# Optimization experiments

Hardware: AMD Instinct MI355X
Metric: run time of the kernel (lower is better)

The kernel has to match this reference:

```python
import jax, jax.numpy as jnp
import numpy as np

B, S, C, L, E, A, H = 4, 4, 4, 512, 64, 32, 8


def _xavier(k, shape, fan_in, fan_out):
    lim = float(np.sqrt(6.0 / (fan_in + fan_out)))
    return jax.random.uniform(k, shape, jnp.float32, -lim, lim)


def setup_inputs() -> dict:
    key = jax.random.key(0)
    ks = jax.random.split(key, 14)
    inp = {
        "query_sequences": jax.random.normal(ks[0], (B, S, L, E), jnp.float32),
        "key_sequences": jax.random.normal(ks[1], (B, S, L, E), jnp.float32),
        "value_sequences": jax.random.normal(ks[2], (B, S, L, E), jnp.float32),
        "query_constants": jax.random.normal(ks[3], (B, C, 1, E), jnp.float32),
        "key_constants": jax.random.normal(ks[4], (B, C, 1, E), jnp.float32),
        "value_constants": jax.random.normal(ks[5], (B, C, 1, E), jnp.float32),
        "qw_seq": _xavier(ks[6], (S, H, E, A), E, A),
        "kw_seq": _xavier(ks[7], (S, H, E, A), E, A),
        "vw_seq": _xavier(ks[8], (S, H, E, A), E, A),
        "qw_con": _xavier(ks[9], (C, H, E, A), E, A),
        "kw_con": _xavier(ks[10], (C, H, E, A), E, A),
        "vw_con": _xavier(ks[11], (C, H, E, A), E, A),
        "head_w_seq": _xavier(ks[12], (S, H * A, E), H * A, E),
        "head_w_con": _xavier(ks[13], (C, H * A, E), H * A, E),
        "mask": 1,
    }
    return inp


def reference(query_sequences, key_sequences, value_sequences,
              query_constants, key_constants, value_constants,
              qw_seq, kw_seq, vw_seq, qw_con, kw_con, vw_con,
              head_w_seq, head_w_con, mask):
    # Per-sequence / per-constant, per-head QKV projections
    q_s = jnp.einsum('bsle,shea->bshla', query_sequences, qw_seq)      # [B,S,H,L,A]
    q_c = jnp.einsum('bcle,chea->bchla', query_constants, qw_con)      # [B,C,H,1,A]
    k_s = jnp.einsum('bsle,shea->bhsla', key_sequences, kw_seq).reshape(B, H, S * L, A)
    k_c = jnp.einsum('bcle,chea->bhcla', key_constants, kw_con).reshape(B, H, C, A)
    v_s = jnp.einsum('bsle,shea->bhsla', value_sequences, vw_seq).reshape(B, H, S * L, A)
    v_c = jnp.einsum('bcle,chea->bhcla', value_constants, vw_con).reshape(B, H, C, A)
    k_all = jnp.concatenate([k_s, k_c], axis=2)                        # [B,H,K,A], K=S*L+C
    v_all = jnp.concatenate([v_s, v_c], axis=2)

    scale = 1.0 / jnp.sqrt(jnp.asarray(A, jnp.float32))
    scores_s = jnp.einsum('bshla,bhka->bshlk', q_s, k_all) * scale     # [B,S,H,L,K]
    if mask:
        # block-causal: within each of the S key blocks mask future timesteps;
        # constant columns (time index -1) are always visible.
        kt = jnp.concatenate([jnp.tile(jnp.arange(L), S), jnp.full((C,), -1)])
        m = kt[None, :] > jnp.arange(L)[:, None]                       # [L,K]
        scores_s = jnp.where(m, -jnp.inf, scores_s)
    p_s = jax.nn.softmax(scores_s, axis=-1)
    out_s = jnp.einsum('bshlk,bhka->bslha', p_s, v_all).reshape(B, S, L, H * A)
    seq_out = jnp.einsum('bslf,sfe->bsle', out_s, head_w_seq)          # [B,S,L,E]

    scores_c = jnp.einsum('bchla,bhka->bchlk', q_c, k_all) * scale     # [B,C,H,1,K]
    p_c = jax.nn.softmax(scores_c, axis=-1)
    out_c = jnp.einsum('bchlk,bhka->bclha', p_c, v_all).reshape(B, C, 1, H * A)
    con_out = jnp.einsum('bclf,cfe->bcle', out_c, head_w_con)          # [B,C,1,E]
    return (seq_out, con_out)
```

## Files before the change

### kernel.cpp

```cpp
#include <hip/hip_runtime.h>
#include <hip/hip_bf16.h>

#define B_ 4
#define S_ 4
#define C_ 4
#define L_ 512
#define E_ 64
#define A_ 32
#define H_ 8
#define HA_ 256
#define KREAL 2052
#define KP 2112
#define NKT 33
#define SCALE 0.17677669529663687f
#define SCALE2 0.25503486321392056f
#define NEGINF (-__builtin_inff())

using bf16  = __bf16;
using bf16x8 = __attribute__((ext_vector_type(8))) __bf16;
using f32x4  = __attribute__((ext_vector_type(4))) float;

#define OFF_QS    0ull
#define OFF_KALL  4194304ull
#define OFF_VT    8519680ull
#define OFF_OUTS  12845056ull
#define OFF_OUTC  17039360ull

__device__ __forceinline__ bool detect_f32(const unsigned int* __restrict__ x0,
                                           int* sh_cnt)
{
  if (threadIdx.x == 0) *sh_cnt = 0;
  __syncthreads();
  int weird = 0;
  for (int i = threadIdx.x; i < 1024; i += blockDim.x) {
    unsigned h = x0[i] & 0xffffu;
    int e = (int)((h >> 7) & 0xFF);
    if (e == 0xFF || e < 0x60 || e > 0x9F) weird++;
  }
  atomicAdd(sh_cnt, weird);
  __syncthreads();
  int cnt = *sh_cnt;
  return __builtin_amdgcn_readfirstlane(cnt) > 256;
}

__device__ __forceinline__ bf16x8 ld8(const void* p, size_t idx, bool isf32) {
  if (isf32) {
    const float* f = (const float*)p + idx;
    float4 lo = *(const float4*)f;
    float4 hi = *(const float4*)(f + 4);
    bf16x8 v;
    v[0] = (bf16)lo.x; v[1] = (bf16)lo.y; v[2] = (bf16)lo.z; v[3] = (bf16)lo.w;
    v[4] = (bf16)hi.x; v[5] = (bf16)hi.y; v[6] = (bf16)hi.z; v[7] = (bf16)hi.w;
    return v;
  }
  return *(const bf16x8*)((const bf16*)p + idx);
}
__device__ __forceinline__ float ldf(const void* p, size_t idx, bool isf32) {
  return isf32 ? ((const float*)p)[idx] : (float)((const bf16*)p)[idx];
}

__global__ __launch_bounds__(256) void proj_kernel(
    const void* __restrict__ xq, const void* __restrict__ xk, const void* __restrict__ xv,
    const void* __restrict__ kc_in, const void* __restrict__ vc_in,
    const void* __restrict__ wq, const void* __restrict__ wk, const void* __restrict__ wv,
    const void* __restrict__ wkc, const void* __restrict__ wvc,
    bf16* __restrict__ qs, bf16* __restrict__ kall, bf16* __restrict__ vt)
{
  __shared__ int sh_cnt;
  bool isf32 = detect_f32((const unsigned int*)xq, &sh_cnt);
  int bid = blockIdx.x;
  int tid = threadIdx.x;
  if (bid < 256) {
    int b = bid >> 6, s = (bid >> 4) & 3, h = (bid >> 1) & 7, lc = bid & 1;
    __shared__ bf16 wt[3 * 32 * 72];
    __shared__ bf16 v_lds[32 * 264];
    {
      size_t hb = (size_t)(s * H_ + h) * E_ * A_;
      int e = tid >> 2, ac = tid & 3;
      bf16x8 vq = ld8(wq, hb + e * 32 + ac * 8, isf32);
      bf16x8 vk = ld8(wk, hb + e * 32 + ac * 8, isf32);
      bf16x8 vv = ld8(wv, hb + e * 32 + ac * 8, isf32);
#pragma unroll
      for (int j = 0; j < 8; ++j) {
        int a = ac * 8 + j;
        wt[0 * 2304 + a * 72 + e] = vq[j];
        wt[1 * 2304 + a * 72 + e] = vk[j];
        wt[2 * 2304 + a * 72 + e] = vv[j];
      }
    }
    __syncthreads();
    int lane = tid & 63, wave = tid >> 6;
    int quad = lane >> 4, r = lane & 15;
    bf16x8 bq[2][2], bk[2][2], bv[2][2];
#pragma unroll
    for (int kc = 0; kc < 2; ++kc)
#pragma unroll
      for (int nt = 0; nt < 2; ++nt) {
        int off = (nt * 16 + r) * 72 + kc * 32 + quad * 8;
        bq[kc][nt] = *(const bf16x8*)&wt[off];
        bk[kc][nt] = *(const bf16x8*)&wt[2304 + off];
        bv[kc][nt] = *(const bf16x8*)&wt[4608 + off];
      }
    const size_t xbase = (size_t)(b * S_ + s) * L_ * E_;
    const size_t qsb   = (size_t)((b * S_ + s) * H_ + h) * L_ * A_;
    const size_t kab   = (size_t)(b * H_ + h) * KP * A_;
    const size_t vtb   = (size_t)(b * H_ + h) * A_ * KP;
#pragma unroll 1
    for (int i = 0; i < 4; ++i) {
      int lloc0 = (wave * 4 + i) * 16;
      int row0 = lc * 256 + lloc0;
      size_t rowoff = xbase + (size_t)(row0 + r) * E_ + quad * 8;
      bf16x8 aq0 = ld8(xq, rowoff, isf32);
      bf16x8 aq1 = ld8(xq, rowoff + 32, isf32);
      bf16x8 ak0 = ld8(xk, rowoff, isf32);
      bf16x8 ak1 = ld8(xk, rowoff + 32, isf32);
      bf16x8 av0 = ld8(xv, rowoff, isf32);
      bf16x8 av1 = ld8(xv, rowoff + 32, isf32);
#pragma unroll
      for (int nt = 0; nt < 2; ++nt) {
        f32x4 accq = {0.f,0.f,0.f,0.f}, acck = {0.f,0.f,0.f,0.f}, accv = {0.f,0.f,0.f,0.f};
        accq = __builtin_amdgcn_mfma_f32_16x16x32_bf16(aq0, bq[0][nt], accq, 0,0,0);
        accq = __builtin_amdgcn_mfma_f32_16x16x32_bf16(aq1, bq[1][nt], accq, 0,0,0);
        acck = __builtin_amdgcn_mfma_f32_16x16x32_bf16(ak0, bk[0][nt], acck, 0,0,0);
        acck = __builtin_amdgcn_mfma_f32_16x16x32_bf16(ak1, bk[1][nt], acck, 0,0,0);
        accv = __builtin_amdgcn_mfma_f32_16x16x32_bf16(av0, bv[0][nt], accv, 0,0,0);
        accv = __builtin_amdgcn_mfma_f32_16x16x32_bf16(av1, bv[1][nt], accv, 0,0,0);
#pragma unroll
        for (int reg = 0; reg < 4; ++reg) {
          int l = row0 + quad * 4 + reg;
          int a = nt * 16 + r;
          qs[qsb + (size_t)l * A_ + a]              = (bf16)(accq[reg] * SCALE2);
          kall[kab + (size_t)(s * L_ + l) * A_ + a] = (bf16)acck[reg];
          v_lds[a * 264 + lloc0 + quad * 4 + reg]   = (bf16)accv[reg];
        }
      }
    }
    __syncthreads();
    {
      int a = tid >> 3, c8 = tid & 7;
      size_t rb = vtb + (size_t)a * KP + s * L_ + lc * 256;
#pragma unroll
      for (int j = 0; j < 4; ++j) {
        int chunk = j * 8 + c8;
        *(bf16x8*)&vt[rb + chunk * 8] = *(const bf16x8*)&v_lds[a * 264 + chunk * 8];
      }
    }
  } else {
    int cid = bid - 256;
    int b = cid >> 5, c = (cid >> 3) & 3, h = cid & 7;
    if (tid < 32) {
      int a = tid;
      float kacc = 0.f, vacc = 0.f;
#pragma unroll 8
      for (int e = 0; e < E_; ++e) {
        float xke = ldf(kc_in, (b * C_ + c) * E_ + e, isf32);
        float xve = ldf(vc_in, (b * C_ + c) * E_ + e, isf32);
        float wke = ldf(wkc, ((size_t)(c * H_ + h) * E_ + e) * A_ + a, isf32);
        float wve = ldf(wvc, ((size_t)(c * H_ + h) * E_ + e) * A_ + a, isf32);
        kacc += xke * wke;
        vacc += xve * wve;
      }
      kall[((size_t)(b * H_ + h) * KP + (S_ * L_ + c)) * A_ + a] = (bf16)kacc;
      vt[((size_t)(b * H_ + h) * A_ + a) * KP + (S_ * L_ + c)]   = (bf16)vacc;
    }
    if (c == 0) {
      for (int idx = tid; idx < 60 * 32; idx += 256) {
        int k = KREAL + (idx >> 5), a = idx & 31;
        kall[((size_t)(b * H_ + h) * KP + k) * A_ + a] = (bf16)0.f;
        vt[((size_t)(b * H_ + h) * A_ + a) * KP + k]   = (bf16)0.f;
      }
    }
  }
}

__global__ __launch_bounds__(256) void attn_kernel(
    const bf16* __restrict__ qs, const bf16* __restrict__ kall, const bf16* __restrict__ vt,
    const int* __restrict__ maskp, bf16* __restrict__ outs,
    const void* __restrict__ qc_raw, const void* __restrict__ wqc_raw,
    const unsigned int* __restrict__ x0, float* __restrict__ outc)
{
  __shared__ __attribute__((aligned(16))) bf16 kt_lds[64 * 40];
  __shared__ __attribute__((aligned(16))) bf16 vt_lds[32 * 72];
  __shared__ __attribute__((aligned(16))) bf16 p_lds[4 * 16 * 72];
  __shared__ int sh_cnt;
  int bid = blockIdx.x, tid = threadIdx.x;
  int lane = tid & 63, wave = tid >> 6, quad = lane >> 4, r = lane & 15;
  if (bid < 1024) {
    int h = bid & 7;
    int q0 = (bid >> 3) & 7;
    int s = (bid >> 6) & 3;
    int b = (bid >> 8) & 3;
    int base = (q0 + 2 * (b >> 1)) & 7;
    int qt = (b & 1) ? 7 - base : base;
    bool causal = (*maskp != 0);
    int wrow = qt * 64 + wave * 16;
    int lrow = wrow + r;
    int blockmax = qt * 64 + 63;

    const size_t qsb = (size_t)((b * S_ + s) * H_ + h) * L_ * A_;
    bf16x8 aq = *(const bf16x8*)&qs[qsb + (size_t)(wrow + r) * A_ + quad * 8];

    f32x4 o[2];
    { f32x4 z = {0.f,0.f,0.f,0.f}; o[0] = z; o[1] = z; }
    float l_run = 0.f;

    const size_t kbase = (size_t)(b * H_ + h) * KP * A_;
    const size_t vbase = (size_t)(b * H_ + h) * A_ * KP;
    const int pbase = wave * 16 * 72;

#pragma unroll 1
    for (int kt = 0; kt < NKT; ++kt) {
      int kmod = (kt & 7) * 64;
      if (causal && kt < 32 && kmod > blockmax) continue;
      __syncthreads();
      {
        int krow = tid >> 2, c4 = tid & 3;
        *(bf16x8*)&kt_lds[krow * 40 + c4 * 8] =
            *(const bf16x8*)&kall[kbase + (size_t)(kt * 64 + krow) * A_ + c4 * 8];
        int a8 = tid >> 3, c8 = tid & 7;
        *(bf16x8*)&vt_lds[a8 * 72 + c8 * 8] =
            *(const bf16x8*)&vt[vbase + (size_t)a8 * KP + kt * 64 + c8 * 8];
      }
      __syncthreads();
      if (causal && kt < 32 && kmod >= wrow + 16) continue;
      bool fullv = (kt < 32) && (!causal || kmod + 63 <= wrow);

      f32x4 sf[4];
#pragma unroll
      for (int kg = 0; kg < 4; ++kg) {
        bf16x8 ka = *(const bf16x8*)&kt_lds[(kg * 16 + r) * 40 + quad * 8];
        f32x4 z = {0.f,0.f,0.f,0.f};
        sf[kg] = __builtin_amdgcn_mfma_f32_16x16x32_bf16(ka, aq, z, 0,0,0);
      }
      if (!fullv) {
        int thresh = (kt < 32) ? (lrow - kmod) : 3;
#pragma unroll
        for (int kg = 0; kg < 4; ++kg)
#pragma unroll
          for (int reg = 0; reg < 4; ++reg)
            if (kg * 16 + quad * 4 + reg > thresh) sf[kg][reg] = NEGINF;
      }
      float psum = 0.f;
#pragma unroll
      for (int kg = 0; kg < 4; ++kg) {
        float p0 = exp2f(sf[kg][0]);
        float p1 = exp2f(sf[kg][1]);
        float p2 = exp2f(sf[kg][2]);
        float p3 = exp2f(sf[kg][3]);
        psum += (p0 + p1) + (p2 + p3);
        union { bf16 hh[4]; uint2 u2; } pk;
        pk.hh[0] = (bf16)p0; pk.hh[1] = (bf16)p1; pk.hh[2] = (bf16)p2; pk.hh[3] = (bf16)p3;
        *(uint2*)&p_lds[pbase + r * 72 + kg * 16 + quad * 4] = pk.u2;
      }
      psum += __shfl_xor(psum, 16);
      psum += __shfl_xor(psum, 32);
      l_run += psum;
#pragma unroll
      for (int kc2 = 0; kc2 < 2; ++kc2) {
        bf16x8 ap = *(const bf16x8*)&p_lds[pbase + r * 72 + kc2 * 32 + quad * 8];
#pragma unroll
        for (int nt = 0; nt < 2; ++nt) {
          bf16x8 bv = *(const bf16x8*)&vt_lds[(nt * 16 + r) * 72 + kc2 * 32 + quad * 8];
          o[nt] = __builtin_amdgcn_mfma_f32_16x16x32_bf16(ap, bv, o[nt], 0,0,0);
        }
      }
    }
    const size_t obase = (size_t)(b * S_ + s) * L_ * HA_;
#pragma unroll
    for (int reg = 0; reg < 4; ++reg) {
      float lo = __shfl(l_run, (lane & 48) | (quad * 4 + reg));
      int orow = wrow + quad * 4 + reg;
#pragma unroll
      for (int nt = 0; nt < 2; ++nt) {
        int f = h * A_ + nt * 16 + r;
        outs[obase + (size_t)orow * HA_ + f] = (bf16)(o[nt][reg] / lo);
      }
    }
  } else {
    bool isf32 = detect_f32(x0, &sh_cnt);
    float* parr  = (float*)p_lds;
    float* qsh   = (float*)kt_lds;
    float* red   = (float*)kt_lds + 64;
    float* opart = (float*)kt_lds + 128;
    int cid = bid - 1024;
    int b = cid >> 5, c = (cid >> 3) & 3, h = cid & 7;
    if (tid < 32) {
      float acc = 0.f;
#pragma unroll 8
      for (int e = 0; e < E_; ++e)
        acc += ldf(qc_raw, (b * C_ + c) * E_ + e, isf32) *
               ldf(wqc_raw, ((size_t)(c * H_ + h) * E_ + e) * A_ + tid, isf32);
      qsh[tid] = acc * SCALE;
    }
    if (tid >= 192 && tid < 192 + (KP - KREAL)) parr[KREAL + tid - 192] = 0.f;
    __syncthreads();
    const size_t kbase = (size_t)(b * H_ + h) * KP * A_;
    float lmax = -1e30f;
#pragma unroll 1
    for (int j = 0; j < 9; ++j) {
      int k = tid + j * 256;
      if (k < KREAL) {
        bf16x8 k0 = *(const bf16x8*)&kall[kbase + (size_t)k * A_ + 0];
        bf16x8 k1 = *(const bf16x8*)&kall[kbase + (size_t)k * A_ + 8];
        bf16x8 k2 = *(const bf16x8*)&kall[kbase + (size_t)k * A_ + 16];
        bf16x8 k3 = *(const bf16x8*)&kall[kbase + (size_t)k * A_ + 24];
        float d = 0.f;
#pragma unroll
        for (int i = 0; i < 8; ++i) {
          d += qsh[i]      * (float)k0[i];
          d += qsh[8 + i]  * (float)k1[i];
          d += qsh[16 + i] * (float)k2[i];
          d += qsh[24 + i] * (float)k3[i];
        }
        parr[k] = d;
        lmax = fmaxf(lmax, d);
      }
    }
#pragma unroll
    for (int dlt = 1; dlt < 64; dlt <<= 1) lmax = fmaxf(lmax, __shfl_xor(lmax, dlt));
    if (lane == 0) red[wave] = lmax;
    __syncthreads();
    float bmax = fmaxf(fmaxf(red[0], red[1]), fmaxf(red[2], red[3]));
    float lsum = 0.f;
#pragma unroll 1
    for (int j = 0; j < 9; ++j) {
      int k = tid + j * 256;
      if (k < KREAL) {
        float p = __expf(parr[k] - bmax);
        parr[k] = p;
        lsum += p;
      }
    }
#pragma unroll
    for (int dlt = 1; dlt < 64; dlt <<= 1) lsum += __shfl_xor(lsum, dlt);
    if (lane == 0) red[4 + wave] = lsum;
    __syncthreads();
    float bsum = (red[4] + red[5]) + (red[6] + red[7]);
    int a = tid >> 3, ch = tid & 7;
    const size_t vbase = (size_t)(b * H_ + h) * A_ * KP + (size_t)a * KP;
    float acc = 0.f;
#pragma unroll 1
    for (int j = 0; j < 33; ++j) {
      int kb = ch * 8 + j * 64;
      bf16x8 vv = *(const bf16x8*)&vt[vbase + kb];
      float4 p0 = *(float4*)&parr[kb];
      float4 p1 = *(float4*)&parr[kb + 4];
      acc += p0.x * (float)vv[0] + p0.y * (float)vv[1] + p0.z * (float)vv[2] + p0.w * (float)vv[3];
      acc += p1.x * (float)vv[4] + p1.y * (float)vv[5] + p1.z * (float)vv[6] + p1.w * (float)vv[7];
    }
    opart[a * 9 + ch] = acc;
    __syncthreads();
    if (tid < 32) {
      float t = 0.f;
#pragma unroll
      for (int i = 0; i < 8; ++i) t += opart[tid * 9 + i];
      outc[(size_t)(b * C_ + c) * HA_ + h * A_ + tid] = t / bsum;
    }
  }
}

__global__ __launch_bounds__(256) void hproj_kernel(
    const bf16* __restrict__ outs, const float* __restrict__ outc,
    const void* __restrict__ hws_raw, const void* __restrict__ hwc_raw,
    const unsigned int* __restrict__ x0, void* __restrict__ out)
{
  __shared__ __attribute__((aligned(16))) bf16 wt[64 * 264];
  __shared__ int sh_cnt;
  bool isf32 = detect_f32(x0, &sh_cnt);
  int bid = blockIdx.x, tid = threadIdx.x;
  if (bid < 128) {
    int b = bid >> 5, s = (bid >> 3) & 3, rc = bid & 7;
    for (int idx = tid; idx < HA_ * E_ / 8; idx += 256) {
      int f = idx >> 3, ec = idx & 7;
      bf16x8 v = ld8(hws_raw, (size_t)s * HA_ * E_ + (size_t)f * E_ + ec * 8, isf32);
#pragma unroll
      for (int j = 0; j < 8; ++j) wt[(ec * 8 + j) * 264 + f] = v[j];
    }
    __syncthreads();
    int lane = tid & 63, wave = tid >> 6, quad = lane >> 4, r = lane & 15;
    int row0 = rc * 64 + wave * 16;
    const size_t xbase = (size_t)(b * S_ + s) * L_ * HA_;
    bf16x8 af[8];
#pragma unroll
    for (int kc = 0; kc < 8; ++kc)
      af[kc] = *(const bf16x8*)&outs[xbase + (size_t)(row0 + r) * HA_ + kc * 32 + quad * 8];
#pragma unroll
    for (int nt = 0; nt < 4; ++nt) {
      f32x4 acc = {0.f,0.f,0.f,0.f};
#pragma unroll
      for (int kc = 0; kc < 8; ++kc) {
        bf16x8 bfr = *(const bf16x8*)&wt[(nt * 16 + r) * 264 + kc * 32 + quad * 8];
        acc = __builtin_amdgcn_mfma_f32_16x16x32_bf16(af[kc], bfr, acc, 0,0,0);
      }
#pragma unroll
      for (int reg = 0; reg < 4; ++reg) {
        int row = row0 + quad * 4 + reg;
        int e = nt * 16 + r;
        size_t oidx = ((size_t)(b * S_ + s) * L_ + row) * E_ + e;
        if (isf32) ((float*)out)[oidx] = acc[reg];
        else       ((bf16*)out)[oidx]  = (bf16)acc[reg];
      }
    }
  } else {
    float* opart = (float*)wt;
    int i2 = bid - 128;
    int b = i2 >> 2, c = i2 & 3;
    int fc = tid >> 6, e = tid & 63;
    const float* oc = outc + (size_t)(b * C_ + c) * HA_;
    float acc = 0.f;
#pragma unroll 4
    for (int fo = 0; fo < 64; ++fo) {
      int f = fc * 64 + fo;
      acc += oc[f] * ldf(hwc_raw, ((size_t)c * HA_ + f) * E_ + e, isf32);
    }
    opart[fc * 68 + e] = acc;
    __syncthreads();
    if (tid < 64) {
      float t = (opart[0 * 68 + tid] + opart[1 * 68 + tid]) +
                (opart[2 * 68 + tid] + opart[3 * 68 + tid]);
      size_t oidx = (size_t)B_ * S_ * L_ * E_ + (size_t)(b * C_ + c) * E_ + tid;
      if (isf32) ((float*)out)[oidx] = t;
      else       ((bf16*)out)[oidx]  = (bf16)t;
    }
  }
}

extern "C" void kernel_launch(void* const* d_in, const int* in_sizes, int n_in,
                              void* d_out, int out_size, void* d_ws, size_t ws_size,
                              hipStream_t stream) {
  char* ws = (char*)d_ws;
  bf16* qs    = (bf16*)(ws + OFF_QS);
  bf16* kall  = (bf16*)(ws + OFF_KALL);
  bf16* vt    = (bf16*)(ws + OFF_VT);
  bf16* outs  = (bf16*)(ws + OFF_OUTS);
  float* outc = (float*)(ws + OFF_OUTC);
  const int* maskp = (const int*)d_in[14];
  const unsigned int* x0 = (const unsigned int*)d_in[0];

  proj_kernel<<<384, 256, 0, stream>>>(d_in[0], d_in[1], d_in[2], d_in[4], d_in[5],
                                       d_in[6], d_in[7], d_in[8], d_in[10], d_in[11],
                                       qs, kall, vt);
  attn_kernel<<<1152, 256, 0, stream>>>(qs, kall, vt, maskp, outs,
                                        d_in[3], d_in[9], x0, outc);
  hproj_kernel<<<144, 256, 0, stream>>>(outs, outc, d_in[12], d_in[13], x0, d_out);
}
```

Measured before the change: 159.5 us.

## Split projection and head kernels into more blocks; use ballot-based dtype detection

The QKV projection kernel now launches 1024 sequence blocks of 64 rows each instead of 256 blocks of 256 rows. The head projection kernel now splits work into 512 blocks of 32 rows by half of E. Both changes aim to fill all CUs on the chip instead of leaving most idle. The dtype detection now reads only 64 words with a wave ballot instead of a block-wide shared-memory atomic reduction, removing two barriers per block. In exchange, the weight staging into LDS is repeated across many more blocks, and the detection rests on a smaller sample.

```diff
diff --git a/kernel.cpp b/kernel.cpp
--- a/kernel.cpp
+++ b/kernel.cpp
@@ -26,21 +26,13 @@
 #define OFF_OUTS  12845056ull
 #define OFF_OUTC  17039360ull
 
-__device__ __forceinline__ bool detect_f32(const unsigned int* __restrict__ x0,
-                                           int* sh_cnt)
+__device__ __forceinline__ bool detect_f32_fast(const unsigned int* __restrict__ x0)
 {
-  if (threadIdx.x == 0) *sh_cnt = 0;
-  __syncthreads();
-  int weird = 0;
-  for (int i = threadIdx.x; i < 1024; i += blockDim.x) {
-    unsigned h = x0[i] & 0xffffu;
-    int e = (int)((h >> 7) & 0xFF);
-    if (e == 0xFF || e < 0x60 || e > 0x9F) weird++;
-  }
-  atomicAdd(sh_cnt, weird);
-  __syncthreads();
-  int cnt = *sh_cnt;
-  return __builtin_amdgcn_readfirstlane(cnt) > 256;
+  unsigned v = x0[threadIdx.x & 63];
+  int e = (int)((v >> 7) & 0xFF);
+  bool weird = (e == 0xFF || e < 0x60 || e > 0x9F);
+  unsigned long long m = __ballot(weird);
+  return __builtin_popcountll(m) > 16;
 }
 
 __device__ __forceinline__ bf16x8 ld8(const void* p, size_t idx, bool isf32) {
@@ -66,14 +58,13 @@
     const void* __restrict__ wkc, const void* __restrict__ wvc,
     bf16* __restrict__ qs, bf16* __restrict__ kall, bf16* __restrict__ vt)
 {
-  __shared__ int sh_cnt;
-  bool isf32 = detect_f32((const unsigned int*)xq, &sh_cnt);
+  bool isf32 = detect_f32_fast((const unsigned int*)xq);
   int bid = blockIdx.x;
   int tid = threadIdx.x;
-  if (bid < 256) {
-    int b = bid >> 6, s = (bid >> 4) & 3, h = (bid >> 1) & 7, lc = bid & 1;
+  if (bid < 1024) {
+    int h = bid & 7, lc8 = (bid >> 3) & 7, s = (bid >> 6) & 3, b = (bid >> 8) & 3;
     __shared__ bf16 wt[3 * 32 * 72];
-    __shared__ bf16 v_lds[32 * 264];
+    __shared__ bf16 v_lds[32 * 72];
     {
       size_t hb = (size_t)(s * H_ + h) * E_ * A_;
       int e = tid >> 2, ac = tid & 3;
@@ -91,62 +82,51 @@
     __syncthreads();
     int lane = tid & 63, wave = tid >> 6;
     int quad = lane >> 4, r = lane & 15;
-    bf16x8 bq[2][2], bk[2][2], bv[2][2];
-#pragma unroll
-    for (int kc = 0; kc < 2; ++kc)
-#pragma unroll
-      for (int nt = 0; nt < 2; ++nt) {
-        int off = (nt * 16 + r) * 72 + kc * 32 + quad * 8;
-        bq[kc][nt] = *(const bf16x8*)&wt[off];
-        bk[kc][nt] = *(const bf16x8*)&wt[2304 + off];
-        bv[kc][nt] = *(const bf16x8*)&wt[4608 + off];
-      }
     const size_t xbase = (size_t)(b * S_ + s) * L_ * E_;
     const size_t qsb   = (size_t)((b * S_ + s) * H_ + h) * L_ * A_;
     const size_t kab   = (size_t)(b * H_ + h) * KP * A_;
     const size_t vtb   = (size_t)(b * H_ + h) * A_ * KP;
-#pragma unroll 1
-    for (int i = 0; i < 4; ++i) {
-      int lloc0 = (wave * 4 + i) * 16;
-      int row0 = lc * 256 + lloc0;
-      size_t rowoff = xbase + (size_t)(row0 + r) * E_ + quad * 8;
-      bf16x8 aq0 = ld8(xq, rowoff, isf32);
-      bf16x8 aq1 = ld8(xq, rowoff + 32, isf32);
-      bf16x8 ak0 = ld8(xk, rowoff, isf32);
-      bf16x8 ak1 = ld8(xk, rowoff + 32, isf32);
-      bf16x8 av0 = ld8(xv, rowoff, isf32);
-      bf16x8 av1 = ld8(xv, rowoff + 32, isf32);
-#pragma unroll
-      for (int nt = 0; nt < 2; ++nt) {
-        f32x4 accq = {0.f,0.f,0.f,0.f}, acck = {0.f,0.f,0.f,0.f}, accv = {0.f,0.f,0.f,0.f};
-        accq = __builtin_amdgcn_mfma_f32_16x16x32_bf16(aq0, bq[0][nt], accq, 0,0,0);
-        accq = __builtin_amdgcn_mfma_f32_16x16x32_bf16(aq1, bq[1][nt], accq, 0,0,0);
-        acck = __builtin_amdgcn_mfma_f32_16x16x32_bf16(ak0, bk[0][nt], acck, 0,0,0);
-        acck = __builtin_amdgcn_mfma_f32_16x16x32_bf16(ak1, bk[1][nt], acck, 0,0,0);
-        accv = __builtin_amdgcn_mfma_f32_16x16x32_bf16(av0, bv[0][nt], accv, 0,0,0);
-        accv = __builtin_amdgcn_mfma_f32_16x16x32_bf16(av1, bv[1][nt], accv, 0,0,0);
-#pragma unroll
-        for (int reg = 0; reg < 4; ++reg) {
-          int l = row0 + quad * 4 + reg;
-          int a = nt * 16 + r;
-          qs[qsb + (size_t)l * A_ + a]              = (bf16)(accq[reg] * SCALE2);
-          kall[kab + (size_t)(s * L_ + l) * A_ + a] = (bf16)acck[reg];
-          v_lds[a * 264 + lloc0 + quad * 4 + reg]   = (bf16)accv[reg];
-        }
+    int lloc0 = wave * 16;
+    int row0 = lc8 * 64 + lloc0;
+    size_t rowoff = xbase + (size_t)(row0 + r) * E_ + quad * 8;
+    bf16x8 aq0 = ld8(xq, rowoff, isf32);
+    bf16x8 aq1 = ld8(xq, rowoff + 32, isf32);
+    bf16x8 ak0 = ld8(xk, rowoff, isf32);
+    bf16x8 ak1 = ld8(xk, rowoff + 32, isf32);
+    bf16x8 av0 = ld8(xv, rowoff, isf32);
+    bf16x8 av1 = ld8(xv, rowoff + 32, isf32);
+#pragma unroll
+    for (int nt = 0; nt < 2; ++nt) {
+      bf16x8 bq0 = *(const bf16x8*)&wt[(nt * 16 + r) * 72 + 0 + quad * 8];
+      bf16x8 bq1 = *(const bf16x8*)&wt[(nt * 16 + r) * 72 + 32 + quad * 8];
+      bf16x8 bk0 = *(const bf16x8*)&wt[2304 + (nt * 16 + r) * 72 + 0 + quad * 8];
+      bf16x8 bk1 = *(const bf16x8*)&wt[2304 + (nt * 16 + r) * 72 + 32 + quad * 8];
+      bf16x8 bv0 = *(const bf16x8*)&wt[4608 + (nt * 16 + r) * 72 + 0 + quad * 8];
+      bf16x8 bv1 = *(const bf16x8*)&wt[4608 + (nt * 16 + r) * 72 + 32 + quad * 8];
+      f32x4 accq = {0.f,0.f,0.f,0.f}, acck = {0.f,0.f,0.f,0.f}, accv = {0.f,0.f,0.f,0.f};
+      accq = __builtin_amdgcn_mfma_f32_16x16x32_bf16(aq0, bq0, accq, 0,0,0);
+      accq = __builtin_amdgcn_mfma_f32_16x16x32_bf16(aq1, bq1, accq, 0,0,0);
+      acck = __builtin_amdgcn_mfma_f32_16x16x32_bf16(ak0, bk0, acck, 0,0,0);
+      acck = __builtin_amdgcn_mfma_f32_16x16x32_bf16(ak1, bk1, acck, 0,0,0);
+      accv = __builtin_amdgcn_mfma_f32_16x16x32_bf16(av0, bv0, accv, 0,0,0);
+      accv = __builtin_amdgcn_mfma_f32_16x16x32_bf16(av1, bv1, accv, 0,0,0);
+#pragma unroll
+      for (int reg = 0; reg < 4; ++reg) {
+        int l = row0 + quad * 4 + reg;
+        int a = nt * 16 + r;
+        qs[qsb + (size_t)l * A_ + a]              = (bf16)(accq[reg] * SCALE2);
+        kall[kab + (size_t)(s * L_ + l) * A_ + a] = (bf16)acck[reg];
+        v_lds[a * 72 + lloc0 + quad * 4 + reg]    = (bf16)accv[reg];
       }
     }
     __syncthreads();
     {
       int a = tid >> 3, c8 = tid & 7;
-      size_t rb = vtb + (size_t)a * KP + s * L_ + lc * 256;
-#pragma unroll
-      for (int j = 0; j < 4; ++j) {
-        int chunk = j * 8 + c8;
-        *(bf16x8*)&vt[rb + chunk * 8] = *(const bf16x8*)&v_lds[a * 264 + chunk * 8];
-      }
+      *(bf16x8*)&vt[vtb + (size_t)a * KP + s * L_ + lc8 * 64 + c8 * 8] =
+          *(const bf16x8*)&v_lds[a * 72 + c8 * 8];
     }
   } else {
-    int cid = bid - 256;
+    int cid = bid - 1024;
     int b = cid >> 5, c = (cid >> 3) & 3, h = cid & 7;
     if (tid < 32) {
       int a = tid;
@@ -182,7 +162,6 @@
   __shared__ __attribute__((aligned(16))) bf16 kt_lds[64 * 40];
   __shared__ __attribute__((aligned(16))) bf16 vt_lds[32 * 72];
   __shared__ __attribute__((aligned(16))) bf16 p_lds[4 * 16 * 72];
-  __shared__ int sh_cnt;
   int bid = blockIdx.x, tid = threadIdx.x;
   int lane = tid & 63, wave = tid >> 6, quad = lane >> 4, r = lane & 15;
   if (bid < 1024) {
@@ -277,7 +256,7 @@
       }
     }
   } else {
-    bool isf32 = detect_f32(x0, &sh_cnt);
+    bool isf32 = detect_f32_fast(x0);
     float* parr  = (float*)p_lds;
     float* qsh   = (float*)kt_lds;
     float* red   = (float*)kt_lds + 64;
@@ -364,46 +343,43 @@
     const void* __restrict__ hws_raw, const void* __restrict__ hwc_raw,
     const unsigned int* __restrict__ x0, void* __restrict__ out)
 {
-  __shared__ __attribute__((aligned(16))) bf16 wt[64 * 264];
-  __shared__ int sh_cnt;
-  bool isf32 = detect_f32(x0, &sh_cnt);
+  __shared__ __attribute__((aligned(16))) bf16 wt[32 * 264];
+  bool isf32 = detect_f32_fast(x0);
   int bid = blockIdx.x, tid = threadIdx.x;
-  if (bid < 128) {
-    int b = bid >> 5, s = (bid >> 3) & 3, rc = bid & 7;
-    for (int idx = tid; idx < HA_ * E_ / 8; idx += 256) {
-      int f = idx >> 3, ec = idx & 7;
-      bf16x8 v = ld8(hws_raw, (size_t)s * HA_ * E_ + (size_t)f * E_ + ec * 8, isf32);
+  if (bid < 512) {
+    int eh = bid & 1, rc = (bid >> 1) & 15, s = (bid >> 5) & 3, b = (bid >> 7) & 3;
+    for (int idx = tid; idx < HA_ * 4; idx += 256) {
+      int f = idx >> 2, ec = idx & 3;
+      bf16x8 v = ld8(hws_raw, (size_t)s * HA_ * E_ + (size_t)f * E_ + eh * 32 + ec * 8, isf32);
 #pragma unroll
       for (int j = 0; j < 8; ++j) wt[(ec * 8 + j) * 264 + f] = v[j];
     }
     __syncthreads();
     int lane = tid & 63, wave = tid >> 6, quad = lane >> 4, r = lane & 15;
-    int row0 = rc * 64 + wave * 16;
+    int rowh = wave & 1, ntw = wave >> 1;
+    int row0 = rc * 32 + rowh * 16;
     const size_t xbase = (size_t)(b * S_ + s) * L_ * HA_;
     bf16x8 af[8];
 #pragma unroll
     for (int kc = 0; kc < 8; ++kc)
       af[kc] = *(const bf16x8*)&outs[xbase + (size_t)(row0 + r) * HA_ + kc * 32 + quad * 8];
-#pragma unroll
-    for (int nt = 0; nt < 4; ++nt) {
-      f32x4 acc = {0.f,0.f,0.f,0.f};
-#pragma unroll
-      for (int kc = 0; kc < 8; ++kc) {
-        bf16x8 bfr = *(const bf16x8*)&wt[(nt * 16 + r) * 264 + kc * 32 + quad * 8];
-        acc = __builtin_amdgcn_mfma_f32_16x16x32_bf16(af[kc], bfr, acc, 0,0,0);
-      }
-#pragma unroll
-      for (int reg = 0; reg < 4; ++reg) {
-        int row = row0 + quad * 4 + reg;
-        int e = nt * 16 + r;
-        size_t oidx = ((size_t)(b * S_ + s) * L_ + row) * E_ + e;
-        if (isf32) ((float*)out)[oidx] = acc[reg];
-        else       ((bf16*)out)[oidx]  = (bf16)acc[reg];
-      }
+    f32x4 acc = {0.f,0.f,0.f,0.f};
+#pragma unroll
+    for (int kc = 0; kc < 8; ++kc) {
+      bf16x8 bfr = *(const bf16x8*)&wt[(ntw * 16 + r) * 264 + kc * 32 + quad * 8];
+      acc = __builtin_amdgcn_mfma_f32_16x16x32_bf16(af[kc], bfr, acc, 0,0,0);
+    }
+#pragma unroll
+    for (int reg = 0; reg < 4; ++reg) {
+      int row = row0 + quad * 4 + reg;
+      int e = eh * 32 + ntw * 16 + r;
+      size_t oidx = ((size_t)(b * S_ + s) * L_ + row) * E_ + e;
+      if (isf32) ((float*)out)[oidx] = acc[reg];
+      else       ((bf16*)out)[oidx]  = (bf16)acc[reg];
     }
   } else {
     float* opart = (float*)wt;
-    int i2 = bid - 128;
+    int i2 = bid - 512;
     int b = i2 >> 2, c = i2 & 3;
     int fc = tid >> 6, e = tid & 63;
     const float* oc = outc + (size_t)(b * C_ + c) * HA_;
@@ -437,10 +413,10 @@
   const int* maskp = (const int*)d_in[14];
   const unsigned int* x0 = (const unsigned int*)d_in[0];
 
-  proj_kernel<<<384, 256, 0, stream>>>(d_in[0], d_in[1], d_in[2], d_in[4], d_in[5],
-                                       d_in[6], d_in[7], d_in[8], d_in[10], d_in[11],
-                                       qs, kall, vt);
+  proj_kernel<<<1152, 256, 0, stream>>>(d_in[0], d_in[1], d_in[2], d_in[4], d_in[5],
+                                        d_in[6], d_in[7], d_in[8], d_in[10], d_in[11],
+                                        qs, kall, vt);
   attn_kernel<<<1152, 256, 0, stream>>>(qs, kall, vt, maskp, outs,
                                         d_in[3], d_in[9], x0, outc);
-  hproj_kernel<<<144, 256, 0, stream>>>(outs, outc, d_in[12], d_in[13], x0, d_out);
-}
+  hproj_kernel<<<528, 256, 0, stream>>>(outs, outc, d_in[12], d_in[13], x0, d_out);
+}
```

New measurement: 161.9 us. No clear change (+1.5%).
